# Performance work log

Hardware: AMD Instinct MI355X
Metric: run time of the kernel (lower is better)

Reference implementation:

```python
import jax, jax.numpy as jnp
import numpy as np

B, S, WP = 64, 128, 18          # batch, words/sentence, padded chars/word
K = 3                            # char window size (module constant)
E = 128                          # embedding_dim
H = 256                          # hidden_dim
L = 4                            # cnn out channels (l=4 in module)
V = 50000                        # vocab size
A = 100                          # alphabet size
T = 50                           # tagset size


def setup_inputs() -> dict:
    key = jax.random.key(0)
    ks = jax.random.split(key, 14)
    n = lambda k, *sh: jax.random.normal(k, sh, dtype=jnp.float32) * 0.1
    return {
        "char_ids": jax.random.randint(ks[0], (B, S, WP), 0, A),
        "word_ids": jax.random.randint(ks[1], (B, S), 0, V),
        "char_emb": n(ks[2], A, E),
        "word_emb": n(ks[3], V + 1, E),
        "cnn_w": n(ks[4], L, K * E),
        "cnn_b": n(ks[5], L),
        "wih_f": n(ks[6], 4 * H, E),
        "whh_f": n(ks[7], 4 * H, H),
        "b_f": n(ks[8], 4 * H),
        "wih_b": n(ks[9], 4 * H, E),
        "whh_b": n(ks[10], 4 * H, H),
        "b_b": n(ks[11], 4 * H),
        "out_w": n(ks[12], T, 2 * H),
        "out_b": n(ks[13], T),
    }


def _lstm(x, Wih, Whh, b, reverse):
    # x: [S, B, E] -> hs: [S, B, H]; PyTorch gate order i, f, g, o
    hdim = Whh.shape[1]

    def step(carry, xt):
        h, c = carry
        z = xt @ Wih.T + h @ Whh.T + b
        i, f, g, o = jnp.split(z, 4, axis=-1)
        c = jax.nn.sigmoid(f) * c + jax.nn.sigmoid(i) * jnp.tanh(g)
        h = jax.nn.sigmoid(o) * jnp.tanh(c)
        return (h, c), h

    h0 = jnp.zeros((x.shape[1], hdim), x.dtype)
    _, hs = jax.lax.scan(step, (h0, h0), x, reverse=reverse)
    return hs


def reference(char_ids, word_ids, char_emb, word_emb, cnn_w, cnn_b,
              wih_f, whh_f, b_f, wih_b, whh_b, b_b, out_w, out_b):
    # --- per-word char CNN + max-pool (fully batched over B, S, positions) ---
    ce = char_emb[char_ids]                        # [B, S, WP, E]
    W = WP - (K - 1)                               # window positions per word
    windows = jnp.concatenate([ce[:, :, i:i + W] for i in range(K)], axis=-1)  # [B,S,W,K*E]
    phi = jnp.einsum('bswd,cd->bswc', windows, cnn_w) + cnn_b                  # [B,S,W,L]
    char_reprs = phi.max(axis=2)                   # [B, S, L] (unused by tag path, as in original)

    # --- word embeddings -> BiLSTM -> linear -> log_softmax over seq dim ---
    we = word_emb[word_ids]                        # [B, S, E]
    x = we.transpose(1, 0, 2)                      # [S, B, E]
    hf = _lstm(x, wih_f, whh_f, b_f, reverse=False)
    hb = _lstm(x, wih_b, whh_b, b_b, reverse=True)
    lstm_out = jnp.concatenate([hf, hb], axis=-1).transpose(1, 0, 2)  # [B, S, 2H]
    tag_space = lstm_out @ out_w.T + out_b         # [B, S, T]
    tag_scores = jax.nn.log_softmax(tag_space, axis=1)  # dim=1 as in original
    return tag_scores, char_reprs
```

## Files before the change

kernel.cpp:

```cpp
#include <hip/hip_runtime.h>
#include <hip/hip_bf16.h>

#define B_  64
#define S_  128
#define WP_ 18
#define K_  3
#define E_  128
#define H_  256
#define L_  4
#define T_  50

typedef __hip_bfloat16 bf16;

__device__ __forceinline__ float b2f(bf16 x) { return __bfloat162float(x); }
__device__ __forceinline__ bf16  f2b(float x) { return __float2bfloat16(x); }

__device__ __forceinline__ float fast_sigmoid(float x) {
    return 1.f / (1.f + __expf(-x));
}
__device__ __forceinline__ float fast_tanh(float x) {
    float a = fminf(fmaxf(2.f * x, -30.f), 30.f);
    float e = __expf(a);
    return (e - 1.f) / (e + 1.f);
}
__device__ __forceinline__ unsigned int pack2(float lo, float hi) {
    bf16 l = f2b(lo), h = f2b(hi);
    unsigned short ls = *(unsigned short*)&l, hs = *(unsigned short*)&h;
    return ((unsigned int)hs << 16) | ls;
}

#define DOT2(z, w, h) asm("v_dot2_f32_bf16 %0, %1, %2, %0" : "+v"(z) : "v"(w), "v"(h))
#define PIN4(V_) asm volatile("" : "+v"((V_).x), "+v"((V_).y), "+v"((V_).z), "+v"((V_).w))

__global__ void k_prep(const float* __restrict__ whh_f, const float* __restrict__ whh_b,
                       const float* __restrict__ wih_f, const float* __restrict__ wih_b,
                       unsigned int* __restrict__ wp_f, unsigned int* __restrict__ wp_b,
                       unsigned int* __restrict__ wihT2_f, unsigned int* __restrict__ wihT2_b) {
    int blk = blockIdx.x, t = threadIdx.x;
    if (blk < 1024) {
        const float* src   = (blk < 512) ? whh_f : whh_b;
        unsigned int* dst  = (blk < 512) ? wp_f  : wp_b;
        int d = ((blk & 511) << 8) + t;
        int m = d >> 12, rem = d & 4095;
        int td = rem >> 2, epair = rem & 3, e = epair << 1;
        int i = td >> 2, p = td & 3, g = m >> 3, kk = m & 7;
        int col = (g << 8) + i;
        int k = (p << 6) + (kk << 3) + e;
        float2 sv = *(const float2*)(src + col * 256 + k);
        dst[d] = pack2(sv.x, sv.y);
    } else {
        int id = blk - 1024;
        const float* src  = (id < 256) ? wih_f   : wih_b;
        unsigned int* dst = (id < 256) ? wihT2_f : wihT2_b;
        int d = ((id & 255) << 8) + t;
        int kp = d >> 10, j = d & 1023;
        float2 sv = *(const float2*)(src + j * 128 + 2 * kp);
        dst[d] = pack2(sv.x, sv.y);
    }
}

__global__ void k_input_proj(const int* __restrict__ word_ids,
                             const float* __restrict__ word_emb,
                             const unsigned int* __restrict__ wihT2_f, const float* __restrict__ b_f,
                             const unsigned int* __restrict__ wihT2_b, const float* __restrict__ b_b,
                             bf16* __restrict__ igq_f, bf16* __restrict__ igq_b) {
    int dir = blockIdx.y;
    const unsigned int* wihT2 = dir ? wihT2_b : wihT2_f;
    const float* bb  = dir ? b_b   : b_f;
    bf16* igq        = dir ? igq_b : igq_f;
    __shared__ unsigned int x2[16][64];
    int t  = threadIdx.x;
    int r0 = blockIdx.x * 16;
    for (int u = t; u < 16 * 64; u += 256) {
        int rr = u >> 6, ep = u & 63;
        int r = r0 + rr;
        int s = r >> 6, b = r & 63;
        int wid = word_ids[b * S_ + s];
        float2 ev = *(const float2*)(word_emb + (size_t)wid * E_ + 2 * ep);
        x2[rr][ep] = pack2(ev.x, ev.y);
    }
    __syncthreads();
    int j = t;
    float acc[4][16];
    #pragma unroll
    for (int cj = 0; cj < 4; ++cj) {
        float bv = bb[j + cj * 256];
        #pragma unroll
        for (int rr = 0; rr < 16; ++rr) acc[cj][rr] = bv;
    }
    for (int kp = 0; kp < 64; ++kp) {
        unsigned int wv[4];
        #pragma unroll
        for (int cj = 0; cj < 4; ++cj) wv[cj] = wihT2[kp * 1024 + j + cj * 256];
        #pragma unroll
        for (int rr = 0; rr < 16; ++rr) {
            unsigned int xp = x2[rr][kp];
            #pragma unroll
            for (int cj = 0; cj < 4; ++cj) DOT2(acc[cj][rr], wv[cj], xp);
        }
    }
    #pragma unroll
    for (int rr = 0; rr < 16; ++rr) {
        uint2 w2;
        w2.x = pack2(acc[0][rr], acc[1][rr]);
        w2.y = pack2(acc[2][rr], acc[3][rr]);
        *(uint2*)(igq + (size_t)(r0 + rr) * 1024 + j * 4) = w2;
    }
}

__global__ __launch_bounds__(1024, 4) void k_lstm_cnn(
        const bf16* __restrict__ igq_f, const bf16* __restrict__ igq_b,
        const uint4* __restrict__ wp_f, const uint4* __restrict__ wp_b,
        float* __restrict__ hf, float* __restrict__ hb,
        const int* __restrict__ char_ids, const float* __restrict__ char_emb,
        const float* __restrict__ cnn_w, const float* __restrict__ cnn_b,
        float* __restrict__ out_char) {
    __shared__ uint4 wlds[9216];
    __shared__ __align__(16) unsigned int hpbuf[2][160];

    int t = threadIdx.x;

    if (blockIdx.x < 128) {
        int b   = blockIdx.x & 63;
        int dir = blockIdx.x >> 6;
        const bf16* igq = dir ? igq_b : igq_f;
        const uint4* wp = dir ? wp_b  : wp_f;
        float* hs       = dir ? hb    : hf;

        int i = t >> 2, p = t & 3;

        for (int u = t; u < 9216; u += 1024) wlds[u] = wp[23 * 1024 + u];
        if (t < 320) ((unsigned int*)hpbuf)[t] = 0;
        float c_reg = 0.f;

        uint4 wreg[23];
        #pragma unroll
        for (int m = 0; m < 23; ++m) {
            wreg[m] = wp[m * 1024 + t];
            PIN4(wreg[m]);
        }
        __syncthreads();

        int cur = 0;
        int s0 = dir ? (S_ - 1) : 0;
        uint2 igu = *(const uint2*)&igq[((size_t)s0 * B_ + b) * 1024 + i * 4];

        for (int step = 0; step < S_; ++step) {
            int s = dir ? (S_ - 1 - step) : step;

            float z0 = 0.f, z1 = 0.f, z2 = 0.f, z3 = 0.f;
            if (p == 0) {
                z0 = __uint_as_float(igu.x << 16);
                z1 = __uint_as_float(igu.x & 0xffff0000u);
                z2 = __uint_as_float(igu.y << 16);
                z3 = __uint_as_float(igu.y & 0xffff0000u);
            }
            const char* hpc = (const char*)hpbuf[cur];
            #pragma unroll
            for (int kk = 0; kk < 8; ++kk) {
                uint4 hv = *(const uint4*)(hpc + p * 144 + kk * 16);
                {   uint4 wv = wreg[kk];
                    DOT2(z0, wv.x, hv.x); DOT2(z0, wv.y, hv.y);
                    DOT2(z0, wv.z, hv.z); DOT2(z0, wv.w, hv.w); }
                {   uint4 wv = wreg[8 + kk];
                    DOT2(z1, wv.x, hv.x); DOT2(z1, wv.y, hv.y);
                    DOT2(z1, wv.z, hv.z); DOT2(z1, wv.w, hv.w); }
                {   uint4 wv = (kk < 7) ? wreg[16 + kk] : wlds[t];
                    DOT2(z2, wv.x, hv.x); DOT2(z2, wv.y, hv.y);
                    DOT2(z2, wv.z, hv.z); DOT2(z2, wv.w, hv.w); }
                {   uint4 wv = wlds[(1 + kk) * 1024 + t];
                    DOT2(z3, wv.x, hv.x); DOT2(z3, wv.y, hv.y);
                    DOT2(z3, wv.z, hv.z); DOT2(z3, wv.w, hv.w); }
            }
            if (step + 1 < S_) {
                int sn = dir ? (S_ - 2 - step) : (step + 1);
                igu = *(const uint2*)&igq[((size_t)sn * B_ + b) * 1024 + i * 4];
            }
            z0 += __shfl_xor(z0, 1); z0 += __shfl_xor(z0, 2);
            z1 += __shfl_xor(z1, 1); z1 += __shfl_xor(z1, 2);
            z2 += __shfl_xor(z2, 1); z2 += __shfl_xor(z2, 2);
            z3 += __shfl_xor(z3, 1); z3 += __shfl_xor(z3, 2);
            if (p == 0) {
                float si = fast_sigmoid(z0);
                float sf = fast_sigmoid(z1);
                float tg = fast_tanh(z2);
                float so = fast_sigmoid(z3);
                c_reg = sf * c_reg + si * tg;
                float hn = so * fast_tanh(c_reg);
                hs[((size_t)s * B_ + b) * 256 + i] = hn;
                char* dstb = (char*)hpbuf[cur ^ 1] + (i >> 6) * 144 + ((i >> 1) & 31) * 4 + (i & 1) * 2;
                *(bf16*)dstb = f2b(hn);
            }
            __syncthreads();
            cur ^= 1;
        }
    } else {
        unsigned int* pool_u = (unsigned int*)wlds;
        float*        pool_f = (float*)wlds;
        int blkc = blockIdx.x - 128;

        for (int u = t; u < 4 * 192; u += 1024) {
            int c = u / 192, pe = u % 192;
            pool_u[c * 196 + pe] = pack2(cnn_w[c * 384 + 2 * pe], cnn_w[c * 384 + 2 * pe + 1]);
        }
        if (t < 4) pool_f[784 + t] = cnn_b[t];
        __syncthreads();

        int wv = t >> 6, lane = t & 63;
        unsigned int* cew = pool_u + 800 + wv * 1224;
        int pos = lane >> 2, c = lane & 3;

        #pragma unroll 1
        for (int j = 0; j < 4; ++j) {
            int word = (blkc * 16 + wv) * 4 + j;
            const int* ids = char_ids + word * WP_;
            for (int row = 0; row < WP_; ++row) {
                float2 ev = *(const float2*)(char_emb + (size_t)ids[row] * 128 + 2 * lane);
                cew[row * 68 + lane] = pack2(ev.x, ev.y);
            }
            float acc = 0.f;
            #pragma unroll
            for (int i = 0; i < K_; ++i) {
                const uint4* cr = (const uint4*)(cew + (pos + i) * 68);
                const uint4* wr = (const uint4*)(pool_u + c * 196 + i * 64);
                #pragma unroll
                for (int q = 0; q < 16; ++q) {
                    uint4 cv = cr[q], wq = wr[q];
                    DOT2(acc, wq.x, cv.x); DOT2(acc, wq.y, cv.y);
                    DOT2(acc, wq.z, cv.z); DOT2(acc, wq.w, cv.w);
                }
            }
            acc += pool_f[784 + c];
            #pragma unroll
            for (int off = 4; off < 64; off <<= 1) acc = fmaxf(acc, __shfl_xor(acc, off));
            if (lane < L_) out_char[(size_t)word * L_ + lane] = acc;
        }
    }
}

__global__ void k_tag_linear(const float* __restrict__ hf, const float* __restrict__ hb,
                             const float* __restrict__ out_w, const float* __restrict__ out_b,
                             float* __restrict__ tag) {
    __shared__ unsigned int ow[50 * 257];
    __shared__ unsigned int hv2[8][256];
    int bs0 = blockIdx.x * 8;
    int t = threadIdx.x;
    for (int u = t; u < 12800; u += 512) {
        int tt = u >> 8, kp = u & 255;
        float2 wv = *(const float2*)(out_w + tt * 512 + 2 * kp);
        ow[tt * 257 + kp] = pack2(wv.x, wv.y);
    }
    for (int u = t; u < 8 * 256; u += 512) {
        int w = u >> 8, q = u & 255;
        int bs = bs0 + w;
        int b = bs >> 7, s = bs & 127;
        const float* hsrc = (q < 128) ? hf : hb;
        float2 v = *(const float2*)(hsrc + ((size_t)s * B_ + b) * 256 + 2 * (q & 127));
        hv2[w][q] = pack2(v.x, v.y);
    }
    __syncthreads();
    int w = t >> 6, tt = t & 63;
    if (tt < T_) {
        int bs = bs0 + w;
        int b = bs >> 7, s = bs & 127;
        float acc = out_b[tt];
        const unsigned int* owr = &ow[tt * 257];
        const unsigned int* hvr = hv2[w];
        #pragma unroll 8
        for (int kp = 0; kp < 256; ++kp) DOT2(acc, owr[kp], hvr[kp]);
        tag[((size_t)b * T_ + tt) * S_ + s] = acc;
    }
}

__global__ void k_log_softmax(const float* __restrict__ tag, float* __restrict__ out) {
    int wid  = (blockIdx.x * 256 + threadIdx.x) >> 6;
    int lane = threadIdx.x & 63;
    if (wid >= B_ * T_) return;
    int b = wid / T_, t = wid % T_;
    const float* row = tag + (size_t)wid * S_;
    float v0 = row[lane], v1 = row[lane + 64];
    float m = fmaxf(v0, v1);
    #pragma unroll
    for (int off = 32; off; off >>= 1) m = fmaxf(m, __shfl_xor(m, off));
    float e = expf(v0 - m) + expf(v1 - m);
    #pragma unroll
    for (int off = 32; off; off >>= 1) e += __shfl_xor(e, off);
    float lse = m + logf(e);
    out[((size_t)b * S_ + lane)      * T_ + t] = v0 - lse;
    out[((size_t)b * S_ + lane + 64) * T_ + t] = v1 - lse;
}

extern "C" void kernel_launch(void* const* d_in, const int* in_sizes, int n_in,
                              void* d_out, int out_size, void* d_ws, size_t ws_size,
                              hipStream_t stream) {
    const int*   char_ids = (const int*)d_in[0];
    const int*   word_ids = (const int*)d_in[1];
    const float* char_emb = (const float*)d_in[2];
    const float* word_emb = (const float*)d_in[3];
    const float* cnn_w    = (const float*)d_in[4];
    const float* cnn_b    = (const float*)d_in[5];
    const float* wih_f    = (const float*)d_in[6];
    const float* whh_f    = (const float*)d_in[7];
    const float* b_f      = (const float*)d_in[8];
    const float* wih_b    = (const float*)d_in[9];
    const float* whh_b    = (const float*)d_in[10];
    const float* b_b      = (const float*)d_in[11];
    const float* out_w    = (const float*)d_in[12];
    const float* out_b    = (const float*)d_in[13];
    float* out = (float*)d_out;
    char* ws   = (char*)d_ws;

    size_t o = 0;
    unsigned int* wihT2_f = (unsigned int*)(ws + o); o += (size_t)64 * 1024 * 4;
    unsigned int* wihT2_b = (unsigned int*)(ws + o); o += (size_t)64 * 1024 * 4;
    unsigned int* wp_f    = (unsigned int*)(ws + o); o += (size_t)1024 * 128 * 4;
    unsigned int* wp_b    = (unsigned int*)(ws + o); o += (size_t)1024 * 128 * 4;
    bf16* igq_f  = (bf16*)(ws + o); o += (size_t)S_ * B_ * 1024 * 2;
    bf16* igq_b  = (bf16*)(ws + o); o += (size_t)S_ * B_ * 1024 * 2;
    float* hf    = (float*)(ws + o); o += (size_t)S_ * B_ * 256 * 4;
    float* hb    = (float*)(ws + o); o += (size_t)S_ * B_ * 256 * 4;
    float* tag   = (float*)(ws + o); o += (size_t)B_ * T_ * S_ * 4;

    k_prep<<<1536, 256, 0, stream>>>(whh_f, whh_b, wih_f, wih_b,
                                     wp_f, wp_b, wihT2_f, wihT2_b);
    k_input_proj<<<dim3(512, 2), 256, 0, stream>>>(word_ids, word_emb,
                                                   wihT2_f, b_f, wihT2_b, b_b, igq_f, igq_b);
    k_lstm_cnn<<<256, 1024, 0, stream>>>(igq_f, igq_b,
                                         (const uint4*)wp_f, (const uint4*)wp_b, hf, hb,
                                         char_ids, char_emb, cnn_w, cnn_b,
                                         out + (size_t)B_ * S_ * T_);
    k_tag_linear<<<B_ * S_ / 8, 512, 0, stream>>>(hf, hb, out_w, out_b, tag);
    k_log_softmax<<<(B_ * T_ + 3) / 4, 256, 0, stream>>>(tag, out);
}
```

Baseline: 372.8 us.

## Store LSTM hidden states as packed bf16 and enlarge input-proj and tag tiles

The LSTM now writes hidden states to global memory as packed bf16 pairs copied from the shared-memory h buffer after the barrier, instead of fp32 per lane. This halves hidden-state traffic and removes the pack step in the tag linear kernel. The input projection block processes 32 rows with 512 threads, two gate columns per thread. The tag linear kernel uses 1024-thread blocks covering 16 positions so the out_w staging is amortised over more rows. The extra global store after the barrier sits on the serial recurrence path, and the larger blocks reduce the number of blocks in flight.

After: 374.0 us. Within noise of the previous version (+0.3%).

```diff
diff --git a/kernel.cpp b/kernel.cpp
--- a/kernel.cpp
+++ b/kernel.cpp
@@ -68,10 +68,10 @@
     const unsigned int* wihT2 = dir ? wihT2_b : wihT2_f;
     const float* bb  = dir ? b_b   : b_f;
     bf16* igq        = dir ? igq_b : igq_f;
-    __shared__ unsigned int x2[16][64];
+    __shared__ unsigned int x2[32][64];
     int t  = threadIdx.x;
-    int r0 = blockIdx.x * 16;
-    for (int u = t; u < 16 * 64; u += 256) {
+    int r0 = blockIdx.x * 32;
+    for (int u = t; u < 32 * 64; u += 512) {
         int rr = u >> 6, ep = u & 63;
         int r = r0 + rr;
         int s = r >> 6, b = r & 63;
@@ -80,38 +80,34 @@
         x2[rr][ep] = pack2(ev.x, ev.y);
     }
     __syncthreads();
-    int j = t;
-    float acc[4][16];
+    int j = t & 255, jh = t >> 8;
+    float acc[2][32];
     #pragma unroll
-    for (int cj = 0; cj < 4; ++cj) {
-        float bv = bb[j + cj * 256];
+    for (int c2 = 0; c2 < 2; ++c2) {
+        float bv = bb[j + (2 * jh + c2) * 256];
         #pragma unroll
-        for (int rr = 0; rr < 16; ++rr) acc[cj][rr] = bv;
+        for (int rr = 0; rr < 32; ++rr) acc[c2][rr] = bv;
     }
     for (int kp = 0; kp < 64; ++kp) {
-        unsigned int wv[4];
+        unsigned int wv0 = wihT2[kp * 1024 + j + (2 * jh) * 256];
+        unsigned int wv1 = wihT2[kp * 1024 + j + (2 * jh + 1) * 256];
         #pragma unroll
-        for (int cj = 0; cj < 4; ++cj) wv[cj] = wihT2[kp * 1024 + j + cj * 256];
-        #pragma unroll
-        for (int rr = 0; rr < 16; ++rr) {
+        for (int rr = 0; rr < 32; ++rr) {
             unsigned int xp = x2[rr][kp];
-            #pragma unroll
-            for (int cj = 0; cj < 4; ++cj) DOT2(acc[cj][rr], wv[cj], xp);
+            DOT2(acc[0][rr], wv0, xp);
+            DOT2(acc[1][rr], wv1, xp);
         }
     }
     #pragma unroll
-    for (int rr = 0; rr < 16; ++rr) {
-        uint2 w2;
-        w2.x = pack2(acc[0][rr], acc[1][rr]);
-        w2.y = pack2(acc[2][rr], acc[3][rr]);
-        *(uint2*)(igq + (size_t)(r0 + rr) * 1024 + j * 4) = w2;
-    }
+    for (int rr = 0; rr < 32; ++rr)
+        *(unsigned int*)(igq + (size_t)(r0 + rr) * 1024 + j * 4 + 2 * jh) =
+            pack2(acc[0][rr], acc[1][rr]);
 }
 
 __global__ __launch_bounds__(1024, 4) void k_lstm_cnn(
         const bf16* __restrict__ igq_f, const bf16* __restrict__ igq_b,
         const uint4* __restrict__ wp_f, const uint4* __restrict__ wp_b,
-        float* __restrict__ hf, float* __restrict__ hb,
+        unsigned int* __restrict__ hfp, unsigned int* __restrict__ hbp,
         const int* __restrict__ char_ids, const float* __restrict__ char_emb,
         const float* __restrict__ cnn_w, const float* __restrict__ cnn_b,
         float* __restrict__ out_char) {
@@ -123,9 +119,9 @@
     if (blockIdx.x < 128) {
         int b   = blockIdx.x & 63;
         int dir = blockIdx.x >> 6;
-        const bf16* igq = dir ? igq_b : igq_f;
-        const uint4* wp = dir ? wp_b  : wp_f;
-        float* hs       = dir ? hb    : hf;
+        const bf16* igq  = dir ? igq_b : igq_f;
+        const uint4* wp  = dir ? wp_b  : wp_f;
+        unsigned int* hs = dir ? hbp   : hfp;
 
         int i = t >> 2, p = t & 3;
 
@@ -187,11 +183,14 @@
                 float so = fast_sigmoid(z3);
                 c_reg = sf * c_reg + si * tg;
                 float hn = so * fast_tanh(c_reg);
-                hs[((size_t)s * B_ + b) * 256 + i] = hn;
                 char* dstb = (char*)hpbuf[cur ^ 1] + (i >> 6) * 144 + ((i >> 1) & 31) * 4 + (i & 1) * 2;
                 *(bf16*)dstb = f2b(hn);
             }
             __syncthreads();
+            if (t < 128) {
+                hs[((size_t)s * B_ + b) * 128 + t] =
+                    hpbuf[cur ^ 1][(t >> 5) * 36 + (t & 31)];
+            }
             cur ^= 1;
         }
     } else {
@@ -238,25 +237,25 @@
     }
 }
 
-__global__ void k_tag_linear(const float* __restrict__ hf, const float* __restrict__ hb,
-                             const float* __restrict__ out_w, const float* __restrict__ out_b,
-                             float* __restrict__ tag) {
+__global__ __launch_bounds__(1024) void k_tag_linear(
+        const unsigned int* __restrict__ hfp, const unsigned int* __restrict__ hbp,
+        const float* __restrict__ out_w, const float* __restrict__ out_b,
+        float* __restrict__ tag) {
     __shared__ unsigned int ow[50 * 257];
-    __shared__ unsigned int hv2[8][256];
-    int bs0 = blockIdx.x * 8;
+    __shared__ unsigned int hv[16][256];
+    int bs0 = blockIdx.x * 16;
     int t = threadIdx.x;
-    for (int u = t; u < 12800; u += 512) {
+    for (int u = t; u < 12800; u += 1024) {
         int tt = u >> 8, kp = u & 255;
         float2 wv = *(const float2*)(out_w + tt * 512 + 2 * kp);
         ow[tt * 257 + kp] = pack2(wv.x, wv.y);
     }
-    for (int u = t; u < 8 * 256; u += 512) {
+    for (int u = t; u < 16 * 256; u += 1024) {
         int w = u >> 8, q = u & 255;
         int bs = bs0 + w;
         int b = bs >> 7, s = bs & 127;
-        const float* hsrc = (q < 128) ? hf : hb;
-        float2 v = *(const float2*)(hsrc + ((size_t)s * B_ + b) * 256 + 2 * (q & 127));
-        hv2[w][q] = pack2(v.x, v.y);
+        const unsigned int* src = (q < 128) ? hfp : hbp;
+        hv[w][q] = src[((size_t)s * B_ + b) * 128 + (q & 127)];
     }
     __syncthreads();
     int w = t >> 6, tt = t & 63;
@@ -265,7 +264,7 @@
         int b = bs >> 7, s = bs & 127;
         float acc = out_b[tt];
         const unsigned int* owr = &ow[tt * 257];
-        const unsigned int* hvr = hv2[w];
+        const unsigned int* hvr = hv[w];
         #pragma unroll 8
         for (int kp = 0; kp < 256; ++kp) DOT2(acc, owr[kp], hvr[kp]);
         tag[((size_t)b * T_ + tt) * S_ + s] = acc;
@@ -317,18 +316,18 @@
     unsigned int* wp_b    = (unsigned int*)(ws + o); o += (size_t)1024 * 128 * 4;
     bf16* igq_f  = (bf16*)(ws + o); o += (size_t)S_ * B_ * 1024 * 2;
     bf16* igq_b  = (bf16*)(ws + o); o += (size_t)S_ * B_ * 1024 * 2;
-    float* hf    = (float*)(ws + o); o += (size_t)S_ * B_ * 256 * 4;
-    float* hb    = (float*)(ws + o); o += (size_t)S_ * B_ * 256 * 4;
+    unsigned int* hfp = (unsigned int*)(ws + o); o += (size_t)S_ * B_ * 128 * 4;
+    unsigned int* hbp = (unsigned int*)(ws + o); o += (size_t)S_ * B_ * 128 * 4;
     float* tag   = (float*)(ws + o); o += (size_t)B_ * T_ * S_ * 4;
 
     k_prep<<<1536, 256, 0, stream>>>(whh_f, whh_b, wih_f, wih_b,
                                      wp_f, wp_b, wihT2_f, wihT2_b);
-    k_input_proj<<<dim3(512, 2), 256, 0, stream>>>(word_ids, word_emb,
+    k_input_proj<<<dim3(256, 2), 512, 0, stream>>>(word_ids, word_emb,
                                                    wihT2_f, b_f, wihT2_b, b_b, igq_f, igq_b);
     k_lstm_cnn<<<256, 1024, 0, stream>>>(igq_f, igq_b,
-                                         (const uint4*)wp_f, (const uint4*)wp_b, hf, hb,
+                                         (const uint4*)wp_f, (const uint4*)wp_b, hfp, hbp,
                                          char_ids, char_emb, cnn_w, cnn_b,
                                          out + (size_t)B_ * S_ * T_);
-    k_tag_linear<<<B_ * S_ / 8, 512, 0, stream>>>(hf, hb, out_w, out_b, tag);
+    k_tag_linear<<<B_ * S_ / 16, 1024, 0, stream>>>(hfp, hbp, out_w, out_b, tag);
     k_log_softmax<<<(B_ * T_ + 3) / 4, 256, 0, stream>>>(tag, out);
 }
```
